# Kernel optimization log

Measured on AMD Instinct MI355X. Metric: run time of the kernel, lower is better.

The kernel has to match this reference:

```python
import jax, jax.numpy as jnp
import numpy as np

IOU_THR = 0.5    # cfg.MODEL.BOX_TEACHER.IOU_THR
SCORE_THR = 0.05 # cfg.MODEL.BOX_TEACHER.SCORE_THR
M, N, H, W = 100, 20, 800, 800


def _pairwise_iou(b1, b2):
    # b1: [M,4] xyxy, b2: [N,4] xyxy -> [M,N]
    area1 = (b1[:, 2] - b1[:, 0]) * (b1[:, 3] - b1[:, 1])
    area2 = (b2[:, 2] - b2[:, 0]) * (b2[:, 3] - b2[:, 1])
    lt = jnp.maximum(b1[:, None, :2], b2[None, :, :2])
    rb = jnp.minimum(b1[:, None, 2:], b2[None, :, 2:])
    wh = jnp.clip(rb - lt, 0.0)
    inter = wh[..., 0] * wh[..., 1]
    union = area1[:, None] + area2[None, :] - inter
    return inter / jnp.clip(union, 1e-6)


def _greedy_match(iou, scores):
    # Faithful replica of the sequential greedy loop in pseudo_labeling1,
    # including the original `gtm[j] > 0` (not > -1) availability check.
    m_, n_ = iou.shape
    order = jnp.argsort(-scores)  # descending by score
    gt_ids = jnp.arange(n_)

    def step(carry, i):
        gtm, biou = carry
        row = iou[i]
        valid = (gtm <= 0) & (row >= IOU_THR)
        masked = jnp.where(valid, row, -jnp.inf)
        m = jnp.argmax(masked)  # first max, matching `iou_ < max_iou` tie rule
        found = valid.any() & (scores[i] >= SCORE_THR)
        hit = found & (gt_ids == m)
        gtm = jnp.where(hit, i.astype(gtm.dtype), gtm)
        biou = jnp.where(hit, row[m], biou)
        return (gtm, biou), None

    gtm0 = jnp.full((n_,), -1, dtype=jnp.int32)
    (gtm, biou), _ = jax.lax.scan(step, (gtm0, jnp.zeros((n_,), iou.dtype)), order)
    return gtm, biou


def setup_inputs() -> dict:
    key = jax.random.key(0)
    k1, k2, k3, k4, k5, k6 = jax.random.split(key, 6)
    cxcy = jax.random.uniform(k1, (M, 2), minval=150.0, maxval=650.0)
    wh = jax.random.uniform(k2, (M, 2), minval=60.0, maxval=300.0)
    pred_boxes = jnp.concatenate([cxcy - wh / 2, cxcy + wh / 2], axis=1)
    # GT boxes are perturbed copies of the first N preds so matching fires
    gt_boxes = pred_boxes[:N] + jax.random.normal(k3, (N, 4)) * 8.0
    pred_scores = jax.random.uniform(k4, (M,))
    mask_score = jax.random.uniform(k5, (M,))
    pred_masks = jax.random.uniform(k6, (M, H, W))
    return {
        "pred_boxes": pred_boxes,
        "pred_scores": pred_scores,
        "mask_score": mask_score,
        "pred_masks": pred_masks,
        "gt_boxes": gt_boxes,
    }


def reference(pred_boxes, pred_scores, mask_score, pred_masks, gt_boxes):
    iou = _pairwise_iou(pred_boxes, gt_boxes)          # [M,N]
    gtm, biou = _greedy_match(iou, pred_scores)        # [N], [N]
    matched = gtm > -1
    idx = jnp.where(matched, gtm, 0)
    # gt_masks[gtm>-1] = pred_masks[gtm[gtm>-1]]
    gt_bitmasks = jnp.where(matched[:, None, None], pred_masks[idx], 0.0)  # [N,H,W]
    gt_masks_flags = jnp.where(matched, mask_score[idx], 0.0)              # [N]
    out_pred_scores = jnp.where(matched, pred_scores[idx], 0.0)            # [N]
    return gt_bitmasks, gt_masks_flags, out_pred_scores
```

## Files before the change

### kernel.cpp

```cpp
#include <hip/hip_runtime.h>
#include <stdint.h>

#define M_PRED 100
#define N_GT 20
#define IMG_H 800
#define IMG_W 800
#define IOU_THR_F 0.5f
#define SCORE_THR_F 0.05f

typedef float f32x4 __attribute__((ext_vector_type(4)));

__global__ __launch_bounds__(128) void match_kernel(
    const float* __restrict__ pred_boxes,
    const float* __restrict__ pred_scores,
    const float* __restrict__ mask_score,
    const float* __restrict__ gt_boxes,
    float* __restrict__ out_flags,
    float* __restrict__ out_scores,
    int* __restrict__ gtm_out)
{
    __shared__ float s_iou[M_PRED * N_GT];
    __shared__ float s_pb[M_PRED * 4];
    __shared__ float s_gb[N_GT * 4];
    __shared__ float s_scores[M_PRED];
    __shared__ int   s_order[M_PRED];
    __shared__ int   s_cand[M_PRED];
    __shared__ int   s_order2[M_PRED];
    __shared__ int   s_ncand;

    const int tid = threadIdx.x;

    for (int t = tid; t < M_PRED * 4; t += 128) s_pb[t] = pred_boxes[t];
    if (tid < N_GT * 4) s_gb[tid] = gt_boxes[tid];
    if (tid < M_PRED)   s_scores[tid] = pred_scores[tid];
    __syncthreads();

    for (int t = tid; t < M_PRED * N_GT; t += 128) {
        int i = t / N_GT, j = t - i * N_GT;
        float ax0 = s_pb[i * 4 + 0], ay0 = s_pb[i * 4 + 1];
        float ax1 = s_pb[i * 4 + 2], ay1 = s_pb[i * 4 + 3];
        float bx0 = s_gb[j * 4 + 0], by0 = s_gb[j * 4 + 1];
        float bx1 = s_gb[j * 4 + 2], by1 = s_gb[j * 4 + 3];
        float area1 = (ax1 - ax0) * (ay1 - ay0);
        float area2 = (bx1 - bx0) * (by1 - by0);
        float lx = fmaxf(ax0, bx0), ly = fmaxf(ay0, by0);
        float rx = fminf(ax1, bx1), ry = fminf(ay1, by1);
        float w = fmaxf(rx - lx, 0.0f), h = fmaxf(ry - ly, 0.0f);
        float inter = w * h;
        float uni = area1 + area2 - inter;
        s_iou[t] = inter / fmaxf(uni, 1e-6f);
    }
    __syncthreads();

    if (tid < M_PRED) {
        float si = s_scores[tid];
        int r = 0;
        for (int k = 0; k < M_PRED; ++k) {
            float sk = s_scores[k];
            r += (sk > si || (sk == si && k < tid)) ? 1 : 0;
        }
        s_order[r] = tid;
        float mx = 0.0f;
        for (int j = 0; j < N_GT; ++j) mx = fmaxf(mx, s_iou[tid * N_GT + j]);
        s_cand[tid] = (si >= SCORE_THR_F && mx >= IOU_THR_F) ? 1 : 0;
    }
    __syncthreads();

    if (tid == 0) {
        int cnt = 0;
        for (int r = 0; r < M_PRED; ++r) {
            int i = s_order[r];
            if (s_cand[i]) s_order2[cnt++] = i;
        }
        s_ncand = cnt;
    }
    __syncthreads();

    if (tid < 32) {
        const int lane = tid;
        const bool is_gt = lane < N_GT;
        int gtm_j = -1;
        const int nc = s_ncand;
        for (int r = 0; r < nc; ++r) {
            int icur = s_order2[r];
            float v = is_gt ? s_iou[icur * N_GT + lane] : -1.0f;
            bool valid = is_gt && (gtm_j <= 0) && (v >= IOU_THR_F);
            float x = valid ? v : -1.0f;
            #pragma unroll
            for (int d = 1; d < 32; d <<= 1)
                x = fmaxf(x, __shfl_xor(x, d, 32));
            unsigned long long mb = __ballot(valid && (v == x));
            if (mb != 0ull) {
                int bj = (int)__builtin_ctzll(mb);
                if (lane == bj) gtm_j = icur;
            }
        }
        if (is_gt) {
            gtm_out[lane] = gtm_j;
            bool matched = gtm_j > -1;
            int idx = matched ? gtm_j : 0;
            out_flags[lane]  = matched ? mask_score[idx] : 0.0f;
            out_scores[lane] = matched ? s_scores[idx]   : 0.0f;
        }
    }
}

__global__ __launch_bounds__(256) void scatter_kernel(
    const f32x4* __restrict__ pred_masks,
    const int* __restrict__ gtm,
    f32x4* __restrict__ out)
{
    const int j = blockIdx.y;
    const int idx = blockIdx.x * 256 + threadIdx.x;
    const int per = (IMG_H * IMG_W) / 4;
    int g = gtm[j];
    f32x4 v = {0.0f, 0.0f, 0.0f, 0.0f};
    if (g > -1) v = __builtin_nontemporal_load(&pred_masks[(size_t)g * per + idx]);
    __builtin_nontemporal_store(v, &out[(size_t)j * per + idx]);
}

extern "C" void kernel_launch(void* const* d_in, const int* in_sizes, int n_in,
                              void* d_out, int out_size, void* d_ws, size_t ws_size,
                              hipStream_t stream) {
    const float* pred_boxes  = (const float*)d_in[0];
    const float* pred_scores = (const float*)d_in[1];
    const float* mask_score  = (const float*)d_in[2];
    const float* pred_masks  = (const float*)d_in[3];
    const float* gt_boxes    = (const float*)d_in[4];
    float* out = (float*)d_out;
    int* gtm_ws = (int*)d_ws;

    float* out_flags  = out + (size_t)N_GT * IMG_H * IMG_W;
    float* out_scores = out_flags + N_GT;

    match_kernel<<<1, 128, 0, stream>>>(pred_boxes, pred_scores, mask_score,
                                        gt_boxes, out_flags, out_scores, gtm_ws);

    dim3 grid((IMG_H * IMG_W / 4) / 256, N_GT);
    scatter_kernel<<<grid, dim3(256), 0, stream>>>(
        (const f32x4*)pred_masks, gtm_ws, (f32x4*)out);
}
```

Before: 332.5 us.

## Fuse matching into scatter kernel with redundant per-block matching

Merges the single-block matching kernel and the mask scatter kernel into one launch. Every one of 2048 blocks recomputes IoU, ranking and greedy matching locally, then runs a grid-stride copy loop. The candidate compaction now uses a ballot-based prefix count instead of a serial loop on one thread. The aim is to remove the second launch and the serial dependency between the tiny match kernel and the copy. In exchange every block repeats the matching work before it starts copying.

```diff
diff --git a/kernel.cpp b/kernel.cpp
--- a/kernel.cpp
+++ b/kernel.cpp
@@ -3,56 +3,56 @@
 
 #define M_PRED 100
 #define N_GT 20
-#define IMG_H 800
-#define IMG_W 800
+#define PER4 160000
 #define IOU_THR_F 0.5f
 #define SCORE_THR_F 0.05f
 
 typedef float f32x4 __attribute__((ext_vector_type(4)));
 
-__global__ __launch_bounds__(128) void match_kernel(
+__global__ __launch_bounds__(256) void fused_kernel(
     const float* __restrict__ pred_boxes,
     const float* __restrict__ pred_scores,
     const float* __restrict__ mask_score,
+    const f32x4* __restrict__ pred_masks,
     const float* __restrict__ gt_boxes,
+    f32x4* __restrict__ out_masks,
     float* __restrict__ out_flags,
-    float* __restrict__ out_scores,
-    int* __restrict__ gtm_out)
+    float* __restrict__ out_scores)
 {
     __shared__ float s_iou[M_PRED * N_GT];
-    __shared__ float s_pb[M_PRED * 4];
     __shared__ float s_gb[N_GT * 4];
     __shared__ float s_scores[M_PRED];
     __shared__ int   s_order[M_PRED];
     __shared__ int   s_cand[M_PRED];
     __shared__ int   s_order2[M_PRED];
+    __shared__ int   s_wcnt[2];
     __shared__ int   s_ncand;
+    __shared__ int   s_gtm[N_GT];
 
     const int tid = threadIdx.x;
 
-    for (int t = tid; t < M_PRED * 4; t += 128) s_pb[t] = pred_boxes[t];
     if (tid < N_GT * 4) s_gb[tid] = gt_boxes[tid];
-    if (tid < M_PRED)   s_scores[tid] = pred_scores[tid];
-    __syncthreads();
-
-    for (int t = tid; t < M_PRED * N_GT; t += 128) {
-        int i = t / N_GT, j = t - i * N_GT;
-        float ax0 = s_pb[i * 4 + 0], ay0 = s_pb[i * 4 + 1];
-        float ax1 = s_pb[i * 4 + 2], ay1 = s_pb[i * 4 + 3];
-        float bx0 = s_gb[j * 4 + 0], by0 = s_gb[j * 4 + 1];
-        float bx1 = s_gb[j * 4 + 2], by1 = s_gb[j * 4 + 3];
-        float area1 = (ax1 - ax0) * (ay1 - ay0);
-        float area2 = (bx1 - bx0) * (by1 - by0);
-        float lx = fmaxf(ax0, bx0), ly = fmaxf(ay0, by0);
-        float rx = fminf(ax1, bx1), ry = fminf(ay1, by1);
-        float w = fmaxf(rx - lx, 0.0f), h = fmaxf(ry - ly, 0.0f);
-        float inter = w * h;
-        float uni = area1 + area2 - inter;
-        s_iou[t] = inter / fmaxf(uni, 1e-6f);
-    }
+    if (tid >= 128 && tid < 128 + M_PRED) s_scores[tid - 128] = pred_scores[tid - 128];
     __syncthreads();
 
     if (tid < M_PRED) {
+        f32x4 b = ((const f32x4*)pred_boxes)[tid];
+        float area1 = (b.z - b.x) * (b.w - b.y);
+        float mx = 0.0f;
+        #pragma unroll
+        for (int j = 0; j < N_GT; ++j) {
+            float bx0 = s_gb[j * 4 + 0], by0 = s_gb[j * 4 + 1];
+            float bx1 = s_gb[j * 4 + 2], by1 = s_gb[j * 4 + 3];
+            float area2 = (bx1 - bx0) * (by1 - by0);
+            float lx = fmaxf(b.x, bx0), ly = fmaxf(b.y, by0);
+            float rx = fminf(b.z, bx1), ry = fminf(b.w, by1);
+            float w = fmaxf(rx - lx, 0.0f), h = fmaxf(ry - ly, 0.0f);
+            float inter = w * h;
+            float uni = area1 + area2 - inter;
+            float iou = inter / fmaxf(uni, 1e-6f);
+            s_iou[tid * N_GT + j] = iou;
+            mx = fmaxf(mx, iou);
+        }
         float si = s_scores[tid];
         int r = 0;
         for (int k = 0; k < M_PRED; ++k) {
@@ -60,20 +60,26 @@
             r += (sk > si || (sk == si && k < tid)) ? 1 : 0;
         }
         s_order[r] = tid;
-        float mx = 0.0f;
-        for (int j = 0; j < N_GT; ++j) mx = fmaxf(mx, s_iou[tid * N_GT + j]);
         s_cand[tid] = (si >= SCORE_THR_F && mx >= IOU_THR_F) ? 1 : 0;
     }
     __syncthreads();
 
-    if (tid == 0) {
-        int cnt = 0;
-        for (int r = 0; r < M_PRED; ++r) {
-            int i = s_order[r];
-            if (s_cand[i]) s_order2[cnt++] = i;
-        }
-        s_ncand = cnt;
+    int  i_pred = -1;
+    bool f = false;
+    int  pos = 0;
+    if (tid < 128) {
+        if (tid < M_PRED) { i_pred = s_order[tid]; f = (s_cand[i_pred] != 0); }
+        unsigned long long mb = __ballot(f);
+        int lane = tid & 63;
+        pos = __popcll(mb & ((1ull << lane) - 1ull));
+        if (lane == 0) s_wcnt[tid >> 6] = __popcll(mb);
     }
+    __syncthreads();
+    if (f) {
+        int base = (tid >= 64) ? s_wcnt[0] : 0;
+        s_order2[base + pos] = i_pred;
+    }
+    if (tid == 0) s_ncand = s_wcnt[0] + s_wcnt[1];
     __syncthreads();
 
     if (tid < 32) {
@@ -96,27 +102,28 @@
             }
         }
         if (is_gt) {
-            gtm_out[lane] = gtm_j;
-            bool matched = gtm_j > -1;
-            int idx = matched ? gtm_j : 0;
-            out_flags[lane]  = matched ? mask_score[idx] : 0.0f;
-            out_scores[lane] = matched ? s_scores[idx]   : 0.0f;
+            s_gtm[lane] = gtm_j;
+            if (blockIdx.x == 0) {
+                bool matched = gtm_j > -1;
+                int idx = matched ? gtm_j : 0;
+                out_flags[lane]  = matched ? mask_score[idx] : 0.0f;
+                out_scores[lane] = matched ? s_scores[idx]   : 0.0f;
+            }
         }
     }
-}
+    __syncthreads();
 
-__global__ __launch_bounds__(256) void scatter_kernel(
-    const f32x4* __restrict__ pred_masks,
-    const int* __restrict__ gtm,
-    f32x4* __restrict__ out)
-{
-    const int j = blockIdx.y;
-    const int idx = blockIdx.x * 256 + threadIdx.x;
-    const int per = (IMG_H * IMG_W) / 4;
-    int g = gtm[j];
-    f32x4 v = {0.0f, 0.0f, 0.0f, 0.0f};
-    if (g > -1) v = __builtin_nontemporal_load(&pred_masks[(size_t)g * per + idx]);
-    __builtin_nontemporal_store(v, &out[(size_t)j * per + idx]);
+    const int total = N_GT * PER4;
+    for (int t = blockIdx.x * 256 + tid; t < total; t += gridDim.x * 256) {
+        unsigned ut = (unsigned)t;
+        int j = (int)(ut / PER4);
+        int k = (int)(ut - (unsigned)j * PER4);
+        int g = s_gtm[j];
+        f32x4 v = {0.0f, 0.0f, 0.0f, 0.0f};
+        if (g > -1)
+            v = __builtin_nontemporal_load(&pred_masks[(size_t)g * PER4 + k]);
+        __builtin_nontemporal_store(v, &out_masks[(size_t)j * PER4 + k]);
+    }
 }
 
 extern "C" void kernel_launch(void* const* d_in, const int* in_sizes, int n_in,
@@ -128,15 +135,11 @@
     const float* pred_masks  = (const float*)d_in[3];
     const float* gt_boxes    = (const float*)d_in[4];
     float* out = (float*)d_out;
-    int* gtm_ws = (int*)d_ws;
 
-    float* out_flags  = out + (size_t)N_GT * IMG_H * IMG_W;
+    float* out_flags  = out + (size_t)N_GT * PER4 * 4;
     float* out_scores = out_flags + N_GT;
 
-    match_kernel<<<1, 128, 0, stream>>>(pred_boxes, pred_scores, mask_score,
-                                        gt_boxes, out_flags, out_scores, gtm_ws);
-
-    dim3 grid((IMG_H * IMG_W / 4) / 256, N_GT);
-    scatter_kernel<<<grid, dim3(256), 0, stream>>>(
-        (const f32x4*)pred_masks, gtm_ws, (f32x4*)out);
+    fused_kernel<<<2048, 256, 0, stream>>>(
+        pred_boxes, pred_scores, mask_score, (const f32x4*)pred_masks,
+        gt_boxes, (f32x4*)out, out_flags, out_scores);
 }
```

Result: no change. 334.8 us (+0.7%).
